# Optimization experiments

Measured on AMD Instinct MI355X. Metric: run time of the kernel, lower is better.

Reference implementation:

```python
import jax, jax.numpy as jnp
import numpy as np

BIN_SIZE = 500      # bin_size from __init__
K = 5               # num_neighbors
DIST_MULT = 0.1
MAX_NUM_BINS = 200


def setup_inputs() -> dict:
    key = jax.random.key(0)
    k1, k2 = jax.random.split(key)
    points = jax.random.normal(k1, (2, 5000, 64), dtype=jnp.float32)
    # codebook_random_rotations: [n_features, max_num_bins // 2]
    rotations = jax.random.normal(k2, (64, MAX_NUM_BINS // 2), dtype=jnp.float32)
    return {"points": points, "rotations": rotations}


def reference(points, rotations):
    """Dense equivalent of the batched tf.SparseTensor output [B, N, N].

    tf.sparse.add sums duplicate (src, dst) entries, which scatter-add
    reproduces exactly.
    """
    B, N, F = points.shape
    nbins = N // BIN_SIZE

    # LSH projection: use first nbins//2 rotation columns, mirror with -mul.
    mul = jnp.einsum('bnf,fh->bnh', points, rotations[:, : nbins // 2])
    cmul = jnp.concatenate([mul, -mul], axis=-1)          # [B, N, nbins]
    bin_idx = jnp.argmax(cmul, axis=-1)                   # [B, N]
    # split_indices_to_bins: stable argsort of bin assignment, reshape to bins
    bins_split = jnp.argsort(bin_idx, axis=-1, stable=True).reshape(B, nbins, BIN_SIZE)

    # gather points into bins: [B, nbins, BIN_SIZE, F]
    parts = jnp.take_along_axis(points, bins_split.reshape(B, N, 1), axis=1)
    parts = parts.reshape(B, nbins, BIN_SIZE, F)

    # pairwise_dist within each bin
    na = jnp.sum(parts * parts, axis=-1)                  # [B, nbins, bs]
    gram = jnp.einsum('bgif,bgjf->bgij', parts, parts)    # [B, nbins, bs, bs]
    dm = jnp.sqrt(jnp.maximum(na[..., :, None] - 2.0 * gram + na[..., None, :], 1e-6))
    aff = jnp.exp(-DIST_MULT * dm)                        # [B, nbins, bs, bs]

    # top-k neighbors per point within its bin
    vals, idx = jax.lax.top_k(aff, K)                     # [B, nbins, bs, K]

    # map local bin indices back to global point indices
    dst = jax.vmap(jax.vmap(lambda b, i: b[i]))(bins_split, idx)   # [B, nbins, bs, K]
    src = jnp.broadcast_to(bins_split[..., None], dst.shape)
    b_ix = jnp.broadcast_to(jnp.arange(B)[:, None, None, None], dst.shape)

    # scatter-add (duplicates summed, as in repeated tf.sparse.add)
    out = jnp.zeros((B, N, N), dtype=points.dtype)
    out = out.at[b_ix, src, dst].add(vals)
    return out
```

## Files before the change

kernel.cpp:

```cpp
#include <hip/hip_runtime.h>
#include <cfloat>
#include <cstddef>

#define NBATCH 2
#define NPTS   5000
#define NF     64
#define NB     10
#define BINSZ  500
#define TOPK   5
#define ROTCOLS 100

#define NZ     3500
#define OUT4   (NBATCH * NPTS * NPTS / 4)
#define CPW    63

__global__ __launch_bounds__(256) void bin_norm_zero_k(const float* __restrict__ pts,
                                                       const float* __restrict__ rot,
                                                       int* __restrict__ bin_idx,
                                                       float* __restrict__ na,
                                                       float* __restrict__ out) {
    const int t = threadIdx.x;
    if (blockIdx.x >= 2500) {
        const int z = blockIdx.x - 2500;
        const int chunk = (OUT4 + NZ - 1) / NZ;
        const size_t base = (size_t)z * chunk;
        size_t end = base + chunk; if (end > (size_t)OUT4) end = OUT4;
        float4* o4 = (float4*)out;
        const float4 z4 = make_float4(0.f, 0.f, 0.f, 0.f);
        for (size_t i = base + t; i < end; i += 256) o4[i] = z4;
        return;
    }
    __shared__ float srot[NF * 5];
    for (int i = t; i < NF * 5; i += 256) {
        int f = i / 5, h = i - 5 * f;
        srot[i] = rot[f * ROTCOLS + h];
    }
    __syncthreads();

    int pt   = blockIdx.x * 4 + (t >> 6);
    int lane = t & 63;
    float p  = pts[(size_t)pt * NF + lane];
    float nn = p * p;
    float c0 = p * srot[lane * 5 + 0];
    float c1 = p * srot[lane * 5 + 1];
    float c2 = p * srot[lane * 5 + 2];
    float c3 = p * srot[lane * 5 + 3];
    float c4 = p * srot[lane * 5 + 4];
    #pragma unroll
    for (int off = 32; off > 0; off >>= 1) {
        nn += __shfl_xor(nn, off);
        c0 += __shfl_xor(c0, off);
        c1 += __shfl_xor(c1, off);
        c2 += __shfl_xor(c2, off);
        c3 += __shfl_xor(c3, off);
        c4 += __shfl_xor(c4, off);
    }
    if (lane == 0) {
        float c[5] = {c0, c1, c2, c3, c4};
        float bv = c[0]; int bi = 0;
        #pragma unroll
        for (int h = 1; h < 5; ++h) if (c[h] > bv) { bv = c[h]; bi = h; }
        #pragma unroll
        for (int h = 0; h < 5; ++h) if (-c[h] > bv) { bv = -c[h]; bi = h + 5; }
        bin_idx[pt] = bi;
        na[pt] = nn;
    }
}

__global__ __launch_bounds__(256) void sort_k(const int* __restrict__ bin_idx,
                                              int* __restrict__ order) {
    const int b = blockIdx.x;
    const int t = threadIdx.x;
    const int w = t >> 6, lane = t & 63;
    __shared__ int sh_bin[NPTS];
    __shared__ int sh_hist[256][NB];
    __shared__ int sh_part[NB][16];
    __shared__ int sh_tot[NB + 1];

    for (int i = t; i < NPTS; i += 256) sh_bin[i] = bin_idx[b * NPTS + i];
    #pragma unroll
    for (int h = 0; h < NB; ++h) sh_hist[t][h] = 0;
    __syncthreads();

    const int CH = (NPTS + 255) / 256;
    const int i0 = t * CH;
    const int i1 = (i0 + CH < NPTS) ? (i0 + CH) : NPTS;
    for (int i = i0; i < i1; ++i) sh_hist[t][sh_bin[i]]++;
    __syncthreads();

    if (t < NB * 16) {
        int h = t >> 4, s = t & 15;
        int sum = 0;
        #pragma unroll
        for (int k = 0; k < 16; ++k) sum += sh_hist[s * 16 + k][h];
        sh_part[h][s] = sum;
    }
    __syncthreads();
    if (t < NB) {
        int tot = 0;
        #pragma unroll
        for (int s = 0; s < 16; ++s) tot += sh_part[t][s];
        sh_tot[t + 1] = tot;
    }
    __syncthreads();
    if (t == 0) {
        sh_tot[0] = 0;
        for (int h = 1; h <= NB; ++h) sh_tot[h] += sh_tot[h - 1];
    }
    __syncthreads();

    for (int h = w; h < NB; h += 4) {
        int base = lane * 4;
        int v0 = sh_hist[base + 0][h];
        int v1 = sh_hist[base + 1][h];
        int v2 = sh_hist[base + 2][h];
        int v3 = sh_hist[base + 3][h];
        int lt = v0 + v1 + v2 + v3;
        int x = lt;
        #pragma unroll
        for (int off = 1; off < 64; off <<= 1) {
            int y = __shfl_up(x, off);
            if (lane >= off) x += y;
        }
        int excl = x - lt + sh_tot[h];
        sh_hist[base + 0][h] = excl;
        sh_hist[base + 1][h] = excl + v0;
        sh_hist[base + 2][h] = excl + v0 + v1;
        sh_hist[base + 3][h] = excl + v0 + v1 + v2;
    }
    __syncthreads();

    for (int i = i0; i < i1; ++i) {
        int h = sh_bin[i];
        order[b * NPTS + sh_hist[t][h]++] = i;
    }
}

__global__ __launch_bounds__(512) void pair_merge_inject_k(const float* __restrict__ pts,
                                                           const float* __restrict__ na,
                                                           const int* __restrict__ order,
                                                           float* __restrict__ out) {
    const int bx   = blockIdx.x;
    const int g    = bx >> 3;
    const int rb   = bx & 7;
    const int b    = g / NB;
    const int grp  = g - b * NB;
    const int tid  = threadIdx.x;
    const int w    = tid >> 6;
    const int lane = tid & 63;

    __shared__ float sh_mv[8][64][TOPK];
    __shared__ int   sh_mi[8][64][TOPK];

    const int* ord = order + b * NPTS + grp * BINSZ;
    const float*  pb  = pts + (size_t)b * NPTS * NF;
    const float4* p4  = (const float4*)pb;
    const float*  nab = na + b * NPTS;

    const int prow = rb * 64 + lane;
    const int pcl  = (prow < BINSZ) ? prow : (BINSZ - 1);
    const int gi   = ord[pcl];
    float4 r[16];
    #pragma unroll
    for (int q = 0; q < 16; ++q) r[q] = p4[(size_t)gi * 16 + q];
    const float* rf = (const float*)r;
    const float na_r = nab[gi];

    float tv[TOPK]; int tp[TOPK];
    #pragma unroll
    for (int s = 0; s < TOPK; ++s) { tv[s] = FLT_MAX; tp[s] = 0; }

    const int c_lo = w * CPW;
    const int c_hi = (c_lo + CPW < BINSZ) ? (c_lo + CPW) : BINSZ;
    for (int cj = c_lo; cj < c_hi; ++cj) {
        const int gc = ord[cj];
        const float colv = pb[(size_t)gc * NF + lane];
        const float cna  = nab[gc];
        float acc = 0.f;
        #pragma unroll
        for (int k = 0; k < 64; ++k) {
            float bc = __uint_as_float(__builtin_amdgcn_readlane(__float_as_uint(colv), k));
            acc += rf[k] * bc;
        }
        float d2 = na_r - 2.f * acc + cna;
        if (d2 < tv[TOPK - 1]) {
            tv[TOPK - 1] = d2; tp[TOPK - 1] = cj;
            #pragma unroll
            for (int s = TOPK - 1; s > 0; --s) {
                if (tv[s] < tv[s - 1]) {
                    float fv = tv[s]; tv[s] = tv[s - 1]; tv[s - 1] = fv;
                    int   fi = tp[s]; tp[s] = tp[s - 1]; tp[s - 1] = fi;
                }
            }
        }
    }

    #pragma unroll
    for (int s = 0; s < TOPK; ++s) { sh_mv[w][lane][s] = tv[s]; sh_mi[w][lane][s] = tp[s]; }
    __syncthreads();

    if (tid < 64) {
        const int r_ = tid;
        const int my = rb * 64 + r_;
        if (my < BINSZ) {
            int h[8] = {0, 0, 0, 0, 0, 0, 0, 0};
            const int src = ord[my];
            float* orow = out + ((size_t)b * NPTS + src) * NPTS;
            #pragma unroll
            for (int s = 0; s < TOPK; ++s) {
                float best = sh_mv[0][r_][h[0]]; int bw = 0;
                #pragma unroll
                for (int ww = 1; ww < 8; ++ww) {
                    float v = sh_mv[ww][r_][h[ww]];
                    if (v < best) { best = v; bw = ww; }
                }
                const int j = sh_mi[bw][r_][h[bw]];
                h[bw]++;
                float val = expf(-0.1f * sqrtf(fmaxf(best, 1e-6f)));
                orow[ord[j]] = val;
            }
        }
    }
}

extern "C" void kernel_launch(void* const* d_in, const int* in_sizes, int n_in,
                              void* d_out, int out_size, void* d_ws, size_t ws_size,
                              hipStream_t stream) {
    const float* points = (const float*)d_in[0];
    const float* rot    = (const float*)d_in[1];
    float* out = (float*)d_out;

    char* ws = (char*)d_ws;
    int*   bin_idx = (int*)ws;   ws += NBATCH * NPTS * sizeof(int);
    float* na      = (float*)ws; ws += NBATCH * NPTS * sizeof(float);
    int*   order   = (int*)ws;

    bin_norm_zero_k<<<2500 + NZ, 256, 0, stream>>>(points, rot, bin_idx, na, out);
    sort_k<<<NBATCH, 256, 0, stream>>>(bin_idx, order);
    pair_merge_inject_k<<<NBATCH * NB * 8, 512, 0, stream>>>(points, na, order, out);
}
```

Measured before the change: 104.4 us.

## Fuse LSH binning and counting sort into the output-zeroing kernel

Merges the per-point projection/norm kernel and the per-batch counting sort into one kernel whose first two blocks compute bins serially per thread and sort, while the remaining blocks zero the output. This removes one kernel launch and the global bin_idx round trip. In exchange, projection for 5000 points now runs on only 256 threads per batch, each thread doing about 20 points with strided float4 loads, which puts a long serial critical path on two blocks.

```diff
diff --git a/kernel.cpp b/kernel.cpp
--- a/kernel.cpp
+++ b/kernel.cpp
@@ -14,14 +14,14 @@
 #define OUT4   (NBATCH * NPTS * NPTS / 4)
 #define CPW    63
 
-__global__ __launch_bounds__(256) void bin_norm_zero_k(const float* __restrict__ pts,
-                                                       const float* __restrict__ rot,
-                                                       int* __restrict__ bin_idx,
-                                                       float* __restrict__ na,
-                                                       float* __restrict__ out) {
+__global__ __launch_bounds__(256) void binsort_zero_k(const float* __restrict__ pts,
+                                                      const float* __restrict__ rot,
+                                                      float* __restrict__ na,
+                                                      int* __restrict__ order,
+                                                      float* __restrict__ out) {
     const int t = threadIdx.x;
-    if (blockIdx.x >= 2500) {
-        const int z = blockIdx.x - 2500;
+    if (blockIdx.x >= NBATCH) {
+        const int z = blockIdx.x - NBATCH;
         const int chunk = (OUT4 + NZ - 1) / NZ;
         const size_t base = (size_t)z * chunk;
         size_t end = base + chunk; if (end > (size_t)OUT4) end = OUT4;
@@ -30,54 +30,19 @@
         for (size_t i = base + t; i < end; i += 256) o4[i] = z4;
         return;
     }
+
+    const int b = blockIdx.x;
+    const int w = t >> 6, lane = t & 63;
+    __shared__ int   sh_bin[NPTS];
+    __shared__ int   sh_hist[256][NB];
+    __shared__ int   sh_part[NB][16];
+    __shared__ int   sh_tot[NB + 1];
     __shared__ float srot[NF * 5];
+
     for (int i = t; i < NF * 5; i += 256) {
         int f = i / 5, h = i - 5 * f;
         srot[i] = rot[f * ROTCOLS + h];
     }
-    __syncthreads();
-
-    int pt   = blockIdx.x * 4 + (t >> 6);
-    int lane = t & 63;
-    float p  = pts[(size_t)pt * NF + lane];
-    float nn = p * p;
-    float c0 = p * srot[lane * 5 + 0];
-    float c1 = p * srot[lane * 5 + 1];
-    float c2 = p * srot[lane * 5 + 2];
-    float c3 = p * srot[lane * 5 + 3];
-    float c4 = p * srot[lane * 5 + 4];
-    #pragma unroll
-    for (int off = 32; off > 0; off >>= 1) {
-        nn += __shfl_xor(nn, off);
-        c0 += __shfl_xor(c0, off);
-        c1 += __shfl_xor(c1, off);
-        c2 += __shfl_xor(c2, off);
-        c3 += __shfl_xor(c3, off);
-        c4 += __shfl_xor(c4, off);
-    }
-    if (lane == 0) {
-        float c[5] = {c0, c1, c2, c3, c4};
-        float bv = c[0]; int bi = 0;
-        #pragma unroll
-        for (int h = 1; h < 5; ++h) if (c[h] > bv) { bv = c[h]; bi = h; }
-        #pragma unroll
-        for (int h = 0; h < 5; ++h) if (-c[h] > bv) { bv = -c[h]; bi = h + 5; }
-        bin_idx[pt] = bi;
-        na[pt] = nn;
-    }
-}
-
-__global__ __launch_bounds__(256) void sort_k(const int* __restrict__ bin_idx,
-                                              int* __restrict__ order) {
-    const int b = blockIdx.x;
-    const int t = threadIdx.x;
-    const int w = t >> 6, lane = t & 63;
-    __shared__ int sh_bin[NPTS];
-    __shared__ int sh_hist[256][NB];
-    __shared__ int sh_part[NB][16];
-    __shared__ int sh_tot[NB + 1];
-
-    for (int i = t; i < NPTS; i += 256) sh_bin[i] = bin_idx[b * NPTS + i];
     #pragma unroll
     for (int h = 0; h < NB; ++h) sh_hist[t][h] = 0;
     __syncthreads();
@@ -85,7 +50,30 @@
     const int CH = (NPTS + 255) / 256;
     const int i0 = t * CH;
     const int i1 = (i0 + CH < NPTS) ? (i0 + CH) : NPTS;
-    for (int i = i0; i < i1; ++i) sh_hist[t][sh_bin[i]]++;
+    const float4* p4 = (const float4*)(pts + (size_t)b * NPTS * NF);
+
+    for (int i = i0; i < i1; ++i) {
+        float nn = 0.f, c0 = 0.f, c1 = 0.f, c2 = 0.f, c3 = 0.f, c4 = 0.f;
+        #pragma unroll
+        for (int q = 0; q < 16; ++q) {
+            float4 v = p4[(size_t)i * 16 + q];
+            const float* s0 = &srot[(4 * q) * 5];
+            nn += v.x * v.x; nn += v.y * v.y; nn += v.z * v.z; nn += v.w * v.w;
+            c0 += v.x * s0[0];  c1 += v.x * s0[1];  c2 += v.x * s0[2];  c3 += v.x * s0[3];  c4 += v.x * s0[4];
+            c0 += v.y * s0[5];  c1 += v.y * s0[6];  c2 += v.y * s0[7];  c3 += v.y * s0[8];  c4 += v.y * s0[9];
+            c0 += v.z * s0[10]; c1 += v.z * s0[11]; c2 += v.z * s0[12]; c3 += v.z * s0[13]; c4 += v.z * s0[14];
+            c0 += v.w * s0[15]; c1 += v.w * s0[16]; c2 += v.w * s0[17]; c3 += v.w * s0[18]; c4 += v.w * s0[19];
+        }
+        na[b * NPTS + i] = nn;
+        float c[5] = {c0, c1, c2, c3, c4};
+        float bv = c[0]; int bi = 0;
+        #pragma unroll
+        for (int h = 1; h < 5; ++h) if (c[h] > bv) { bv = c[h]; bi = h; }
+        #pragma unroll
+        for (int h = 0; h < 5; ++h) if (-c[h] > bv) { bv = -c[h]; bi = h + 5; }
+        sh_bin[i] = bi;
+        sh_hist[t][bi]++;
+    }
     __syncthreads();
 
     if (t < NB * 16) {
@@ -231,11 +219,9 @@
     float* out = (float*)d_out;
 
     char* ws = (char*)d_ws;
-    int*   bin_idx = (int*)ws;   ws += NBATCH * NPTS * sizeof(int);
-    float* na      = (float*)ws; ws += NBATCH * NPTS * sizeof(float);
-    int*   order   = (int*)ws;
-
-    bin_norm_zero_k<<<2500 + NZ, 256, 0, stream>>>(points, rot, bin_idx, na, out);
-    sort_k<<<NBATCH, 256, 0, stream>>>(bin_idx, order);
+    float* na    = (float*)ws; ws += NBATCH * NPTS * sizeof(float);
+    int*   order = (int*)ws;
+
+    binsort_zero_k<<<NBATCH + NZ, 256, 0, stream>>>(points, rot, na, order, out);
     pair_merge_inject_k<<<NBATCH * NB * 8, 512, 0, stream>>>(points, na, order, out);
 }
```

After: 134.4 us. 28.7% more time.
